# Optimization experiments

Hardware: AMD Instinct MI355X
Metric: run time of the kernel (lower is better)

The kernel has to match this reference:

```python
import jax, jax.numpy as jnp
import numpy as np


def setup_inputs() -> dict:
    key = jax.random.key(0)
    k1, k2 = jax.random.split(key)
    B, N, Fin, Fout, K = 4, 4096, 64, 64, 20
    x = jax.random.normal(k1, (B, N, Fin), dtype=jnp.float32)
    # nn.Linear(2*Fin, Fout): weight [Fout, 2*Fin], bias [Fout]
    W = jax.random.normal(k2, (Fout, 2 * Fin), dtype=jnp.float32) * (1.0 / np.sqrt(2 * Fin))
    b = jnp.zeros((Fout,), dtype=jnp.float32)
    return {"x": x, "W": W, "b": b, "k": K}


def _edge_features(x, k):
    # x: [B, N, F] -> edge features [B, N, k, 2F]
    # pairwise squared distance: ||xi||^2 - 2 xi.xj + ||xj||^2
    xs = jnp.sum(x * x, axis=2, keepdims=True)            # [B, N, 1]
    dist = xs - 2.0 * jnp.einsum('bnf,bmf->bnm', x, x) + jnp.swapaxes(xs, 1, 2)  # [B, N, N]
    idx = jnp.argsort(dist, axis=2)[:, :, 1:k + 1]        # skip self -> [B, N, k]
    # gather neighbor features per batch (vectorized index_select)
    neighbors = jax.vmap(lambda xb, ib: xb[ib])(x, idx)   # [B, N, k, F]
    central = jnp.broadcast_to(x[:, :, None, :], neighbors.shape)
    return jnp.concatenate([central, neighbors - central], axis=3)  # [B, N, k, 2F]


def reference(x, W, b, k):
    ee = _edge_features(x, k)                 # [B, N, k, 2F]
    h = jnp.einsum('bnkc,oc->bnko', ee, W) + b  # Linear(2F -> Fout)
    return jnp.max(h, axis=2)                 # max over k neighbors -> [B, N, Fout]
```

## Files before the change

### kernel.cpp

```cpp
#include <hip/hip_runtime.h>
#include <float.h>


constexpr int Bb = 4, Nn = 4096, Ff = 64, Kk = 20;

typedef __attribute__((ext_vector_type(8))) short bf16x8;
typedef __attribute__((ext_vector_type(16))) float f32x16;

__device__ inline unsigned int bf16rn(float f) {
  unsigned int u = __float_as_uint(f);
  return (u + 0x7fffu + ((u >> 16) & 1u)) >> 16;
}

constexpr int RT1 = 16;

__global__ __launch_bounds__(256) void uv_kernel2(
    const float* __restrict__ x, const float* __restrict__ W,
    const float* __restrict__ bvec, float* __restrict__ u,
    float* __restrict__ v, float* __restrict__ sq,
    unsigned short* __restrict__ xhi, unsigned short* __restrict__ xlo) {
  __shared__ __align__(16) float4 Ws[64 * 33];
  __shared__ __align__(16) float4 xs[RT1 * 16];
  const int t = threadIdx.x, l = t & 63, w = t >> 6;
  const int bn0 = blockIdx.x * RT1;
  #pragma unroll
  for (int i = 0; i < 8; i++) {
    int f = t + 256 * i;
    Ws[(f >> 5) * 33 + (f & 31)] = ((const float4*)W)[f];
  }
  xs[t] = ((const float4*)x)[bn0 * 16 + t];
  __syncthreads();
  #pragma unroll
  for (int i = 0; i < 4; i++) {
    int idx = t + 256 * i;
    int nloc = idx >> 6;
    int k = idx & 63;
    float val = ((const float*)xs)[idx];
    unsigned int hb = bf16rn(val);
    float fhi = __uint_as_float(hb << 16);
    unsigned int lb = bf16rn(val - fhi);
    int ng = bn0 + nloc;
    size_t flat = ((size_t)(ng >> 5) << 11) + ((size_t)(k >> 4) << 9) +
                  ((size_t)((k >> 3) & 1) << 8) + ((size_t)(ng & 31) << 3) +
                  (size_t)(k & 7);
    xhi[flat] = (unsigned short)hb;
    xlo[flat] = (unsigned short)lb;
  }
  #pragma unroll
  for (int i = 0; i < 4; i++) {
    int r = 4 * w + i;
    float val = ((const float*)&xs[r * 16])[l];
    float s = val * val;
    #pragma unroll
    for (int d = 32; d; d >>= 1) s += __shfl_xor(s, d, 64);
    if (l == 0) sq[bn0 + r] = s;
  }
  const int o = l;
  float ua[4] = {0.f, 0.f, 0.f, 0.f}, va[4] = {0.f, 0.f, 0.f, 0.f};
  #pragma unroll
  for (int c = 0; c < 16; c++) {
    float4 w1 = Ws[o * 33 + c];
    float4 w2 = Ws[o * 33 + 16 + c];
    float4 wd;
    wd.x = w1.x - w2.x; wd.y = w1.y - w2.y;
    wd.z = w1.z - w2.z; wd.w = w1.w - w2.w;
    #pragma unroll
    for (int i = 0; i < 4; i++) {
      float4 xv = xs[(4 * w + i) * 16 + c];
      ua[i] += xv.x * wd.x + xv.y * wd.y + xv.z * wd.z + xv.w * wd.w;
      va[i] += xv.x * w2.x + xv.y * w2.y + xv.z * w2.z + xv.w * w2.w;
    }
  }
  float bo = bvec[o];
  #pragma unroll
  for (int i = 0; i < 4; i++) {
    size_t row = (size_t)(bn0 + 4 * w + i);
    u[row * 64 + o] = ua[i] + bo;
    v[row * 64 + o] = va[i];
  }
}


__global__ __launch_bounds__(256) void key_mfma_kernel(
    const unsigned short* __restrict__ xhi,
    const unsigned short* __restrict__ xlo, const float* __restrict__ sq,
    unsigned short* __restrict__ keys) {
  const int t = threadIdx.x, l = t & 63, w = t >> 6;
  const int blk = blockIdx.x;
  const int b = blk >> 8;
  const int r = blk & 255;
  const int n_base = (r >> 1) * 32;
  const int m0w = (r & 1) * 2048 + w * 512;
  const int col = l & 31, half = l >> 5;

  const unsigned short* xhb = xhi + (size_t)b * Nn * Ff;
  const unsigned short* xlb = xlo + (size_t)b * Nn * Ff;
  const float* sqb = sq + b * Nn;

  bf16x8 Ahi[4], Alo[4];
  #pragma unroll
  for (int ks = 0; ks < 4; ks++) {
    size_t off = ((size_t)((n_base >> 5) * 4 + ks) << 9) + ((size_t)l << 3);
    Ahi[ks] = *(const bf16x8*)(xhb + off);
    Alo[ks] = *(const bf16x8*)(xlb + off);
  }
  float sqn_r[16];
  #pragma unroll
  for (int e = 0; e < 16; e++) {
    int row = (e & 3) + 8 * (e >> 2) + 4 * half;
    sqn_r[e] = sqb[n_base + row];
  }

  for (int j = 0; j < 16; ++j) {
    const int m0 = m0w + 32 * j;
    const int mblk = m0 >> 5;
    bf16x8 Bhi[4], Blo[4];
    #pragma unroll
    for (int ks = 0; ks < 4; ks++) {
      size_t off = ((size_t)(mblk * 4 + ks) << 9) + ((size_t)l << 3);
      Bhi[ks] = *(const bf16x8*)(xhb + off);
      Blo[ks] = *(const bf16x8*)(xlb + off);
    }
    f32x16 acc = {0.f, 0.f, 0.f, 0.f, 0.f, 0.f, 0.f, 0.f,
                  0.f, 0.f, 0.f, 0.f, 0.f, 0.f, 0.f, 0.f};
    #pragma unroll
    for (int ks = 0; ks < 4; ks++) {
      acc = __builtin_amdgcn_mfma_f32_32x32x16_bf16(Ahi[ks], Bhi[ks], acc, 0, 0, 0);
      acc = __builtin_amdgcn_mfma_f32_32x32x16_bf16(Ahi[ks], Blo[ks], acc, 0, 0, 0);
      acc = __builtin_amdgcn_mfma_f32_32x32x16_bf16(Alo[ks], Bhi[ks], acc, 0, 0, 0);
    }
    const int m = m0 + col;
    const float sm = sqb[m];
    #pragma unroll
    for (int e = 0; e < 16; e++) {
      int row = (e & 3) + 8 * (e >> 2) + 4 * half;
      int n = n_base + row;
      float d = fmaxf(sqn_r[e] + sm - 2.0f * acc[e], 0.f);
      unsigned int key = __float_as_uint(d) >> 15;
      if (m == n) key = 0xFFFFu;
      keys[((size_t)(b * Nn + n) << 12) + m] = (unsigned short)key;
    }
  }
}

__global__ __launch_bounds__(256) void select_kernel(
    const float* __restrict__ x, const unsigned short* __restrict__ keys,
    const float* __restrict__ u, const float* __restrict__ v,
    float* __restrict__ out) {
  __shared__ int candS[4 * 64];
  __shared__ int ccntS[4];
  __shared__ unsigned long long keyS[4 * 64];
  const int t = threadIdx.x, l = t & 63, w = t >> 6;
  const int row = blockIdx.x * 4 + w;
  const int rowu = __builtin_amdgcn_readfirstlane(row);
  const int b = rowu >> 12, n = rowu & (Nn - 1);
  const uint4* kr = (const uint4*)(keys + (size_t)rowu * Nn);
  uint4 kv[8];
  #pragma unroll
  for (int j = 0; j < 8; j++) kv[j] = kr[j * 64 + l];

  auto countLE = [&](int mid) -> int {
    int c = 0;
    #pragma unroll
    for (int j = 0; j < 8; j++) {
      unsigned int a0 = kv[j].x, a1 = kv[j].y, a2 = kv[j].z, a3 = kv[j].w;
      c += ((int)(a0 & 0xffffu) <= mid) + ((int)(a0 >> 16) <= mid);
      c += ((int)(a1 & 0xffffu) <= mid) + ((int)(a1 >> 16) <= mid);
      c += ((int)(a2 & 0xffffu) <= mid) + ((int)(a2 >> 16) <= mid);
      c += ((int)(a3 & 0xffffu) <= mid) + ((int)(a3 >> 16) <= mid);
    }
    #pragma unroll
    for (int d2 = 1; d2 < 64; d2 <<= 1) c += __shfl_xor(c, d2, 64);
    return c;
  };

  unsigned int mn = 0xffffffffu;
  #pragma unroll
  for (int j = 0; j < 8; j++) {
    unsigned int a0 = kv[j].x, a1 = kv[j].y, a2 = kv[j].z, a3 = kv[j].w;
    mn = min(mn, min(min(a0 & 0xffffu, a0 >> 16), min(a1 & 0xffffu, a1 >> 16)));
    mn = min(mn, min(min(a2 & 0xffffu, a2 >> 16), min(a3 & 0xffffu, a3 >> 16)));
  }
  #pragma unroll
  for (int d2 = 1; d2 < 64; d2 <<= 1)
    mn = min(mn, (unsigned int)__shfl_xor((int)mn, d2, 64));

  int lo = (int)mn - 1;
  int hi = (int)mn + 64;
  if (hi > 65534) hi = 65534;
  int c = countLE(hi);
  int step = 128;
  while (c < Kk && hi < 65534) {
    lo = hi;
    hi += step;
    if (hi > 65534) hi = 65534;
    step <<= 1;
    c = countLE(hi);
  }
  while (c > 44 && hi - lo > 1) {
    int mid = (lo + hi) >> 1;
    int cm = countLE(mid);
    if (cm >= Kk) { hi = mid; c = cm; } else { lo = mid; }
  }
  const int hc = hi + 1;

  if (l == 0) ccntS[w] = 0;
  #pragma unroll
  for (int j = 0; j < 8; j++) {
    unsigned int a[4] = {kv[j].x, kv[j].y, kv[j].z, kv[j].w};
    #pragma unroll
    for (int e = 0; e < 4; e++) {
      int base = ((j * 64 + l) * 4 + e) * 2;
      if ((int)(a[e] & 0xffffu) <= hc) {
        int slot = atomicAdd(&ccntS[w], 1);
        if (slot < 64) candS[w * 64 + slot] = base;
      }
      if ((int)(a[e] >> 16) <= hc) {
        int slot = atomicAdd(&ccntS[w], 1);
        if (slot < 64) candS[w * 64 + slot] = base + 1;
      }
    }
  }
  int C = ccntS[w];
  if (C > 64) C = 64;

  const float4* xb4 = (const float4*)(x + (size_t)b * Nn * Ff);
  unsigned long long key64 = 0xFFFFFFFF00000000ull | (unsigned int)l;
  if (l < C) {
    int mI = candS[w * 64 + l];
    const float4* xmf = xb4 + (size_t)mI * 16;
    float ds = 0.f;
    #pragma unroll
    for (int cc = 0; cc < 16; cc++) {
      float4 a = xb4[(size_t)n * 16 + cc];
      float4 bb = xmf[cc];
      float dx = a.x - bb.x, dy = a.y - bb.y, dz = a.z - bb.z, dw2 = a.w - bb.w;
      ds += dx * dx + dy * dy + dz * dz + dw2 * dw2;
    }
    if (mI == n) ds = FLT_MAX;
    key64 = ((unsigned long long)__float_as_uint(ds) << 32) | (unsigned int)mI;
  }

  keyS[w * 64 + l] = key64;
  const unsigned long long* kws = &keyS[w * 64];
  int rank = 0;
  #pragma unroll
  for (int j = 0; j < 64; j += 4) {
    rank += (kws[j] < key64) + (kws[j + 1] < key64) +
            (kws[j + 2] < key64) + (kws[j + 3] < key64);
  }
  if (rank < Kk)
    candS[w * 64 + rank] = (int)(key64 & 0xffffffffu) & (Nn - 1);

  const float* vb = v + (size_t)b * Nn * Ff;
  const size_t oidx = (size_t)rowu * 64 + l;
  float uo = u[oidx];
  float vv[Kk];
  #pragma unroll
  for (int i = 0; i < Kk; i++) {
    int mI = candS[w * 64 + i];
    vv[i] = vb[(size_t)mI * 64 + l];
  }
  float vmax = vv[0];
  #pragma unroll
  for (int i = 1; i < Kk; i++) vmax = fmaxf(vmax, vv[i]);
  out[oidx] = uo + vmax;
}

constexpr int RTF = 4;
constexpr int MTF = 64;
constexpr int TPADF = 17;
constexpr int CCAPF = 64;

__global__ __launch_bounds__(256) void knn_kernel(
    const float* __restrict__ x, const float* __restrict__ sq,
    const float* __restrict__ u, const float* __restrict__ v,
    float* __restrict__ out) {
  __shared__ __align__(16) float4 tileS[MTF * TPADF];
  __shared__ __align__(16) unsigned short keysS[RTF * Nn];
  __shared__ int candS[RTF * CCAPF];
  __shared__ int ccntS[RTF];
  const int t = threadIdx.x;
  const int l = t & 63, w = t >> 6;
  const int q = l & 15, g = l >> 4;
  const int bn0 = blockIdx.x * RTF;
  const int b = bn0 >> 12;
  const int n0 = bn0 & (Nn - 1);
  const float4* xb4 = (const float4*)(x + (size_t)b * Nn * Ff);
  const float* sqb = sq + b * Nn;
  if (t < RTF) ccntS[t] = 0;
  float4 xnq[RTF][4];
  #pragma unroll
  for (int r = 0; r < RTF; r++)
    #pragma unroll
    for (int c = 0; c < 4; c++) xnq[r][c] = xb4[(n0 + r) * 16 + 4 * g + c];
  const float sn = sqb[n0 + g];
  const int selfm = n0 + g;
  for (int T = 0; T < Nn / MTF; ++T) {
    __syncthreads();
    #pragma unroll
    for (int i = 0; i < 4; i++) {
      int f = t + 256 * i;
      tileS[(f >> 4) * TPADF + (f & 15)] = xb4[T * 1024 + f];
    }
    __syncthreads();
    const int mrow = 16 * w + q;
    const float4* xmp = &tileS[mrow * TPADF + 4 * g];
    float4 xm0 = xmp[0], xm1 = xmp[1], xm2 = xmp[2], xm3 = xmp[3];
    float dot[RTF];
    #pragma unroll
    for (int r = 0; r < RTF; r++) {
      float4 a0 = xnq[r][0], a1 = xnq[r][1], a2 = xnq[r][2], a3 = xnq[r][3];
      dot[r] = a0.x * xm0.x + a0.y * xm0.y + a0.z * xm0.z + a0.w * xm0.w +
               a1.x * xm1.x + a1.y * xm1.y + a1.z * xm1.z + a1.w * xm1.w +
               a2.x * xm2.x + a2.y * xm2.y + a2.z * xm2.z + a2.w * xm2.w +
               a3.x * xm3.x + a3.y * xm3.y + a3.z * xm3.z + a3.w * xm3.w;
    }
    #pragma unroll
    for (int r = 0; r < RTF; r++) {
      dot[r] += __shfl_xor(dot[r], 16, 64);
      dot[r] += __shfl_xor(dot[r], 32, 64);
    }
    float dg = (g == 0) ? dot[0] : (g == 1) ? dot[1] : (g == 2) ? dot[2] : dot[3];
    int m = T * MTF + mrow;
    float d = fmaxf(fmaf(-2.f, dg, sqb[m] + sn), 0.f);
    unsigned int key = __float_as_uint(d) >> 15;
    if (m == selfm) key = 0xFFFFu;
    keysS[g * Nn + m] = (unsigned short)key;
  }
  __syncthreads();
  const unsigned int* kp = (const unsigned int*)&keysS[w * Nn];
  int lo = -1, hi = 65535, cntHi = Nn;
  while (cntHi > 48 && hi - lo > 1) {
    int mid = (lo + hi) >> 1;
    unsigned int midu = (unsigned int)mid;
    int c = 0;
    #pragma unroll
    for (int cc = 0; cc < 8; ++cc) {
      int rc = (cc + l) & 7;
      uint4 k4 = *(const uint4*)(kp + l * 32 + rc * 4);
      c += ((k4.x & 0xffffu) <= midu) + ((k4.x >> 16) <= midu);
      c += ((k4.y & 0xffffu) <= midu) + ((k4.y >> 16) <= midu);
      c += ((k4.z & 0xffffu) <= midu) + ((k4.z >> 16) <= midu);
      c += ((k4.w & 0xffffu) <= midu) + ((k4.w >> 16) <= midu);
    }
    #pragma unroll
    for (int d2 = 1; d2 < 64; d2 <<= 1) c += __shfl_xor(c, d2, 64);
    if (c >= Kk) { hi = mid; cntHi = c; } else { lo = mid; }
  }
  {
    unsigned int hu = (unsigned int)hi;
    #pragma unroll
    for (int cc = 0; cc < 8; ++cc) {
      int rc = (cc + l) & 7;
      uint4 k4 = *(const uint4*)(kp + l * 32 + rc * 4);
      unsigned int ks[4] = {k4.x, k4.y, k4.z, k4.w};
      #pragma unroll
      for (int uu = 0; uu < 4; ++uu) {
        #pragma unroll
        for (int hh = 0; hh < 2; ++hh) {
          unsigned int kvv = hh ? (ks[uu] >> 16) : (ks[uu] & 0xffffu);
          if (kvv <= hu) {
            int slot = atomicAdd(&ccntS[w], 1);
            if (slot < CCAPF) candS[w * CCAPF + slot] = l * 64 + (rc * 4 + uu) * 2 + hh;
          }
        }
      }
    }
  }
  __syncthreads();
  const int n = n0 + w;
  const int C = min(cntHi, CCAPF);
  unsigned long long key64 = ~0ULL;
  if (l < C) {
    int mI = candS[w * CCAPF + l];
    const float4* xmf = xb4 + mI * 16;
    float ds = 0.f;
    #pragma unroll
    for (int c = 0; c < 16; c++) {
      float4 a = xb4[n * 16 + c];
      float4 bb = xmf[c];
      float dx = a.x - bb.x, dy = a.y - bb.y, dz = a.z - bb.z, dw2 = a.w - bb.w;
      ds += dx * dx + dy * dy + dz * dz + dw2 * dw2;
    }
    key64 = ((unsigned long long)__float_as_uint(ds) << 32) | (unsigned int)mI;
  }
  float vmax = -FLT_MAX;
  const float* vb = v + (size_t)b * Nn * Ff;
  #pragma unroll
  for (int it = 0; it < Kk; ++it) {
    unsigned long long kmin = key64;
    #pragma unroll
    for (int d2 = 1; d2 < 64; d2 <<= 1) {
      unsigned long long o =
          (unsigned long long)__shfl_xor((long long)kmin, d2, 64);
      kmin = (o < kmin) ? o : kmin;
    }
    int mI = (int)(kmin & 0xffffffffu) & (Nn - 1);
    vmax = fmaxf(vmax, vb[(size_t)mI * 64 + l]);
    if (key64 == kmin) key64 = ~0ULL;
  }
  const size_t oidx = (size_t)(bn0 + w) * 64 + l;
  out[oidx] = u[oidx] + vmax;
}

extern "C" void kernel_launch(void* const* d_in, const int* in_sizes, int n_in,
                              void* d_out, int out_size, void* d_ws,
                              size_t ws_size, hipStream_t stream) {
  const float* x = (const float*)d_in[0];
  const float* W = (const float*)d_in[1];
  const float* bvec = (const float*)d_in[2];
  float* u = (float*)d_ws;
  float* v = u + (size_t)Bb * Nn * Ff;
  float* sq = v + (size_t)Bb * Nn * Ff;
  unsigned short* xhi = (unsigned short*)(sq + (size_t)Bb * Nn);
  unsigned short* xlo = xhi + (size_t)Bb * Nn * Ff;
  unsigned short* keys = xlo + (size_t)Bb * Nn * Ff;
  float* out = (float*)d_out;
  const size_t need = (size_t)Bb * Nn * Ff * 4 * 2 + (size_t)Bb * Nn * 4 +
                      (size_t)Bb * Nn * Ff * 2 * 2 + (size_t)Bb * Nn * Nn * 2;

  uv_kernel2<<<Bb * Nn / RT1, 256, 0, stream>>>(x, W, bvec, u, v, sq, xhi, xlo);
  if (ws_size >= need) {
    key_mfma_kernel<<<Bb * Nn / 16, 256, 0, stream>>>(xhi, xlo, sq, keys);
    select_kernel<<<Bb * Nn / 4, 256, 0, stream>>>(x, keys, u, v, out);
  } else {
    knn_kernel<<<Bb * Nn / RTF, 256, 0, stream>>>(x, sq, u, v, out);
  }
}
```

Before: 157.4 us.

## Find kNN key threshold via LDS histogram and compact candidates with ballot

The repeated countLE binary search for the k-th smallest key threshold is replaced by a 256-bin per-wave LDS histogram of keys offset from the row minimum, followed by a wave prefix scan that picks the threshold bin directly. The old search remains as a fallback when fewer than K keys fall inside the 256-bin window. Candidate compaction now uses ballot plus mbcnt in place of per-element LDS atomics. This cuts the many full passes over the 4096 register-held keys, but adds LDS atomic contention on the histogram.

Result: faster. 149.2 us (-5.2%).

```diff
diff --git a/kernel.cpp b/kernel.cpp
--- a/kernel.cpp
+++ b/kernel.cpp
@@ -148,8 +148,8 @@
     const float* __restrict__ u, const float* __restrict__ v,
     float* __restrict__ out) {
   __shared__ int candS[4 * 64];
-  __shared__ int ccntS[4];
   __shared__ unsigned long long keyS[4 * 64];
+  __shared__ unsigned int histS[4][256];
   const int t = threadIdx.x, l = t & 63, w = t >> 6;
   const int row = blockIdx.x * 4 + w;
   const int rowu = __builtin_amdgcn_readfirstlane(row);
@@ -159,6 +159,9 @@
   #pragma unroll
   for (int j = 0; j < 8; j++) kv[j] = kr[j * 64 + l];
 
+  #pragma unroll
+  for (int i = 0; i < 4; i++) histS[w][4 * l + i] = 0u;
+
   auto countLE = [&](int mid) -> int {
     int c = 0;
     #pragma unroll
@@ -185,43 +188,90 @@
   for (int d2 = 1; d2 < 64; d2 <<= 1)
     mn = min(mn, (unsigned int)__shfl_xor((int)mn, d2, 64));
 
-  int lo = (int)mn - 1;
-  int hi = (int)mn + 64;
-  if (hi > 65534) hi = 65534;
-  int c = countLE(hi);
-  int step = 128;
-  while (c < Kk && hi < 65534) {
-    lo = hi;
-    hi += step;
-    if (hi > 65534) hi = 65534;
-    step <<= 1;
-    c = countLE(hi);
-  }
-  while (c > 44 && hi - lo > 1) {
-    int mid = (lo + hi) >> 1;
-    int cm = countLE(mid);
-    if (cm >= Kk) { hi = mid; c = cm; } else { lo = mid; }
-  }
-  const int hc = hi + 1;
-
-  if (l == 0) ccntS[w] = 0;
   #pragma unroll
   for (int j = 0; j < 8; j++) {
     unsigned int a[4] = {kv[j].x, kv[j].y, kv[j].z, kv[j].w};
     #pragma unroll
     for (int e = 0; e < 4; e++) {
-      int base = ((j * 64 + l) * 4 + e) * 2;
-      if ((int)(a[e] & 0xffffu) <= hc) {
-        int slot = atomicAdd(&ccntS[w], 1);
-        if (slot < 64) candS[w * 64 + slot] = base;
+      unsigned int r0 = (a[e] & 0xffffu) - mn;
+      unsigned int r1 = (a[e] >> 16) - mn;
+      if (r0 < 256u) atomicAdd(&histS[w][r0], 1u);
+      if (r1 < 256u) atomicAdd(&histS[w][r1], 1u);
+    }
+  }
+  unsigned int s0 = histS[w][4 * l + 0], s1 = histS[w][4 * l + 1];
+  unsigned int s2 = histS[w][4 * l + 2], s3 = histS[w][4 * l + 3];
+  unsigned int ls = s0 + s1 + s2 + s3;
+  unsigned int cum = ls;
+  #pragma unroll
+  for (int d2 = 1; d2 < 64; d2 <<= 1) {
+    unsigned int o = (unsigned int)__shfl_up((int)cum, d2, 64);
+    cum += (l >= d2) ? o : 0u;
+  }
+  unsigned int excl = cum - ls;
+  unsigned int c0 = excl + s0, c1 = c0 + s1, c2 = c1 + s2;
+  unsigned long long bal = __ballot(cum >= (unsigned int)Kk);
+
+  int hc;
+  if (bal != 0ull) {
+    int b_loc = (c0 >= (unsigned)Kk) ? 0 : (c1 >= (unsigned)Kk) ? 1
+              : (c2 >= (unsigned)Kk) ? 2 : 3;
+    int flane = __ffsll((unsigned long long)bal) - 1;
+    int hi_rel = __shfl(4 * l + b_loc, flane, 64);
+    hc = (int)mn + hi_rel + 1;
+  } else {
+    int lo = (int)mn - 1;
+    int hi = (int)mn + 64;
+    if (hi > 65534) hi = 65534;
+    int c = countLE(hi);
+    int step = 128;
+    while (c < Kk && hi < 65534) {
+      lo = hi;
+      hi += step;
+      if (hi > 65534) hi = 65534;
+      step <<= 1;
+      c = countLE(hi);
+    }
+    while (c > 44 && hi - lo > 1) {
+      int mid = (lo + hi) >> 1;
+      int cm = countLE(mid);
+      if (cm >= Kk) { hi = mid; c = cm; } else { lo = mid; }
+    }
+    hc = hi + 1;
+  }
+
+  int base = 0;
+  #pragma unroll
+  for (int j = 0; j < 8; j++) {
+    unsigned int a[4] = {kv[j].x, kv[j].y, kv[j].z, kv[j].w};
+    #pragma unroll
+    for (int e = 0; e < 4; e++) {
+      int pos = ((j * 64 + l) * 4 + e) * 2;
+      {
+        bool p = (int)(a[e] & 0xffffu) <= hc;
+        unsigned long long m = __ballot(p);
+        if (p) {
+          int slot = base + __builtin_amdgcn_mbcnt_hi(
+                                (unsigned int)(m >> 32),
+                                __builtin_amdgcn_mbcnt_lo((unsigned int)m, 0));
+          if (slot < 64) candS[w * 64 + slot] = pos;
+        }
+        base += __popcll(m);
       }
-      if ((int)(a[e] >> 16) <= hc) {
-        int slot = atomicAdd(&ccntS[w], 1);
-        if (slot < 64) candS[w * 64 + slot] = base + 1;
+      {
+        bool p = (int)(a[e] >> 16) <= hc;
+        unsigned long long m = __ballot(p);
+        if (p) {
+          int slot = base + __builtin_amdgcn_mbcnt_hi(
+                                (unsigned int)(m >> 32),
+                                __builtin_amdgcn_mbcnt_lo((unsigned int)m, 0));
+          if (slot < 64) candS[w * 64 + slot] = pos + 1;
+        }
+        base += __popcll(m);
       }
     }
   }
-  int C = ccntS[w];
+  int C = base;
   if (C > 64) C = 64;
 
   const float4* xb4 = (const float4*)(x + (size_t)b * Nn * Ff);
```
